# Kernel optimization log

Measured on AMD Instinct MI355X. Metric: run time of the kernel, lower is better.

The kernel has to match this reference:

```python
import jax, jax.numpy as jnp
import numpy as np

EPS = 1e-12  # matches torch F.normalize eps


def setup_inputs() -> dict:
    key = jax.random.key(0)
    k_x, k_w, k_b, k_c, k_f = jax.random.split(key, 5)
    N, C, H, W = 32, 128, 64, 64
    K = 64
    x = jax.random.normal(k_x, (N, C, H, W), dtype=jnp.float32)
    conv_w = jax.random.normal(k_w, (K, C), dtype=jnp.float32) * 0.05  # 1x1 conv weight [K,C,1,1] squeezed
    conv_b = jax.random.normal(k_b, (K,), dtype=jnp.float32) * 0.05
    centroids = jax.random.uniform(k_c, (K, C), dtype=jnp.float32)
    fc_w = jax.random.normal(k_f, (1, K), dtype=jnp.float32) * 0.1  # nn.Linear(K,1,bias=False).weight
    return {"x": x, "conv_w": conv_w, "conv_b": conv_b, "centroids": centroids, "fc_w": fc_w}


def _l2norm(v, axis):
    return v / jnp.maximum(jnp.linalg.norm(v, axis=axis, keepdims=True), EPS)


def reference(x, conv_w, conv_b, centroids, fc_w):
    N, C, H, W = x.shape
    K = conv_w.shape[0]
    # descriptor-wise L2 normalize over channel dim
    x = _l2norm(x, axis=1)
    xf = x.reshape(N, C, H * W)                                   # [N,C,S]
    # 1x1 conv == per-pixel linear over channels
    logits = jnp.einsum('kc,ncs->nks', conv_w, xf) + conv_b[None, :, None]
    a = jax.nn.softmax(logits, axis=1)                            # [N,K,S] soft assignment
    # VLAD: sum_s a[n,k,s] * (x[n,:,s] - centroids[k,:]), loop-free
    vlad = jnp.einsum('nks,ncs->nkc', a, xf) \
           - a.sum(axis=-1)[..., None] * centroids[None, :, :]    # [N,K,C]
    # intra-normalization over descriptor dim
    vlad = _l2norm(vlad, axis=2)
    # lastfc: [N,C,K] @ [K] -> [N,C]
    out = jnp.einsum('nkc,k->nc', vlad, fc_w[0])
    return out
```

## Files before the change

kernel.cpp:

```cpp
#include <hip/hip_runtime.h>
#include <math.h>

#define Nn 32
#define Cc 128
#define Ss 4096
#define Kk 64
#define NCHUNK 32
#define SCHUNK (Ss / NCHUNK)
#define ST 64
#define NSUB (SCHUNK / ST)
#define BLK 256

#define XCS 72
#define XTS 136
#define LKS 68
#define AS  72
#define RS  17

typedef __attribute__((ext_vector_type(8))) short short8;
typedef __attribute__((ext_vector_type(4))) float float4v;

__device__ __forceinline__ unsigned f2bf(float f) {
    unsigned u = __builtin_bit_cast(unsigned, f);
    return (u + 0x7fffu + ((u >> 16) & 1u)) >> 16;
}

__device__ __forceinline__ void bar_lds() {
    asm volatile("s_waitcnt lgkmcnt(0)" ::: "memory");
    __builtin_amdgcn_s_barrier();
    asm volatile("" ::: "memory");
}

__global__ __launch_bounds__(BLK, 3) void netvlad_main(
    const float* __restrict__ x,
    const float* __restrict__ conv_w,
    const float* __restrict__ conv_b,
    float* __restrict__ vladp,
    float* __restrict__ asump,
    float* __restrict__ out)
{
    __shared__ __align__(16) unsigned short xC[Cc * XCS];
    __shared__ __align__(16) float Lbuf[ST * LKS];
    __shared__ __align__(16) unsigned short aB[Kk * AS];
    __shared__ float red[ST * RS];
    __shared__ float invn[ST];
    unsigned short* xT = (unsigned short*)Lbuf;

    const int t     = threadIdx.x;
    const int n     = blockIdx.y;
    const int chunk = blockIdx.x;
    const int w    = t >> 6;
    const int l    = t & 63;
    const int m    = l & 15;
    const int quad = l >> 4;
    const int p    = t >> 2;
    const int ii   = t & 3;

    if (chunk == 0 && n == 0) {
        float4 z4 = make_float4(0.f, 0.f, 0.f, 0.f);
#pragma unroll
        for (int i = 0; i < 4; ++i)
            ((float4*)out)[t + 256 * i] = z4;
    }

    short8 wfrag[4];
    {
        const float* wr_ = conv_w + (16 * w + m) * Cc;
#pragma unroll
        for (int ks = 0; ks < 4; ++ks) {
            float4 wa = *(const float4*)(wr_ + 32 * ks + 8 * quad);
            float4 wb = *(const float4*)(wr_ + 32 * ks + 8 * quad + 4);
            union { short8 s8; unsigned u[4]; } W_;
            W_.u[0] = f2bf(wa.x) | (f2bf(wa.y) << 16);
            W_.u[1] = f2bf(wa.z) | (f2bf(wa.w) << 16);
            W_.u[2] = f2bf(wb.x) | (f2bf(wb.y) << 16);
            W_.u[3] = f2bf(wb.z) | (f2bf(wb.w) << 16);
            wfrag[ks] = W_.s8;
        }
    }
    float bias_r[4];
#pragma unroll
    for (int r = 0; r < 4; ++r) bias_r[r] = conv_b[16 * w + 4 * quad + r];

    float4v acc[8];
#pragma unroll
    for (int nt = 0; nt < 8; ++nt) acc[nt] = (float4v){0.f, 0.f, 0.f, 0.f};
    float asum_part[16];
#pragma unroll
    for (int j = 0; j < 16; ++j) asum_part[j] = 0.f;

    const float* xn = x + (size_t)n * Cc * Ss;

    const int sq   = (t & 15) << 2;
    const int crow = t >> 4;
    const float* xbase = xn + (size_t)(8 * crow) * Ss + chunk * SCHUNK + sq;
    float4 pf[8];
#pragma unroll
    for (int r = 0; r < 8; ++r)
        pf[r] = *(const float4*)(xbase + (size_t)r * Ss);

    for (int sub = 0; sub < NSUB; ++sub) {
        bar_lds();

        {
            unsigned bf[8][4];
            float sp0 = 0.f, sp1 = 0.f, sp2 = 0.f, sp3 = 0.f;
#pragma unroll
            for (int r = 0; r < 8; ++r) {
                float4 v = pf[r];
                sp0 += v.x * v.x; sp1 += v.y * v.y;
                sp2 += v.z * v.z; sp3 += v.w * v.w;
                bf[r][0] = f2bf(v.x); bf[r][1] = f2bf(v.y);
                bf[r][2] = f2bf(v.z); bf[r][3] = f2bf(v.w);
            }
#pragma unroll
            for (int r = 0; r < 8; ++r) {
                uint2 pk = make_uint2(bf[r][0] | (bf[r][1] << 16),
                                      bf[r][2] | (bf[r][3] << 16));
                *(uint2*)&xC[(8 * crow + r) * XCS + sq] = pk;
            }
#pragma unroll
            for (int i = 0; i < 4; ++i) {
                uint4 dd;
                dd.x = bf[0][i] | (bf[1][i] << 16);
                dd.y = bf[2][i] | (bf[3][i] << 16);
                dd.z = bf[4][i] | (bf[5][i] << 16);
                dd.w = bf[6][i] | (bf[7][i] << 16);
                *(uint4*)&xT[(sq + i) * XTS + 8 * crow] = dd;
            }
            red[(sq + 0) * RS + crow] = sp0;
            red[(sq + 1) * RS + crow] = sp1;
            red[(sq + 2) * RS + crow] = sp2;
            red[(sq + 3) * RS + crow] = sp3;
        }
        if (sub < NSUB - 1) {
#pragma unroll
            for (int r = 0; r < 8; ++r)
                pf[r] = *(const float4*)(xbase + (size_t)r * Ss + (sub + 1) * ST);
        }
        bar_lds();

        if (t < ST) {
            float tot = 0.f;
#pragma unroll
            for (int i = 0; i < 16; ++i) tot += red[t * RS + i];
            invn[t] = 1.0f / fmaxf(sqrtf(tot), 1e-12f);
        }
        float4v Lr[4];
#pragma unroll
        for (int nt = 0; nt < 4; ++nt) Lr[nt] = (float4v){0.f, 0.f, 0.f, 0.f};
#pragma unroll
        for (int nt = 0; nt < 4; ++nt) {
#pragma unroll
            for (int ks = 0; ks < 4; ++ks) {
                short8 b = *(const short8*)&xT[(16 * nt + m) * XTS + 32 * ks + 8 * quad];
                Lr[nt] = __builtin_amdgcn_mfma_f32_16x16x32_bf16(wfrag[ks], b, Lr[nt], 0, 0, 0);
            }
        }
        bar_lds();

#pragma unroll
        for (int nt = 0; nt < 4; ++nt) {
            float iv = invn[16 * nt + m];
            float4 o;
            o.x = Lr[nt].x * iv + bias_r[0];
            o.y = Lr[nt].y * iv + bias_r[1];
            o.z = Lr[nt].z * iv + bias_r[2];
            o.w = Lr[nt].w * iv + bias_r[3];
            *(float4*)&Lbuf[(16 * nt + m) * LKS + 16 * w + 4 * quad] = o;
        }
        bar_lds();

        {
            float lv[16];
#pragma unroll
            for (int j = 0; j < 16; ++j) lv[j] = Lbuf[p * LKS + ii + 4 * j];
            float mx = lv[0];
#pragma unroll
            for (int j = 1; j < 16; ++j) mx = fmaxf(mx, lv[j]);
            mx = fmaxf(mx, __shfl_xor(mx, 1));
            mx = fmaxf(mx, __shfl_xor(mx, 2));
            float e[16];
            float lsum = 0.f;
#pragma unroll
            for (int j = 0; j < 16; ++j) { e[j] = __expf(lv[j] - mx); lsum += e[j]; }
            lsum += __shfl_xor(lsum, 1);
            lsum += __shfl_xor(lsum, 2);
            float itot = 1.0f / lsum;
            float sca  = itot * invn[p];
#pragma unroll
            for (int j = 0; j < 16; ++j) {
                float av = e[j] * itot;
                asum_part[j] += av;
                aB[(ii + 4 * j) * AS + p] = (unsigned short)f2bf(e[j] * sca);
            }
        }
        bar_lds();

#pragma unroll
        for (int ks = 0; ks < 2; ++ks) {
            short8 af = *(const short8*)&aB[(16 * w + m) * AS + 32 * ks + 8 * quad];
#pragma unroll
            for (int nt = 0; nt < 8; ++nt) {
                short8 bf_ = *(const short8*)&xC[(16 * nt + m) * XCS + 32 * ks + 8 * quad];
                acc[nt] = __builtin_amdgcn_mfma_f32_16x16x32_bf16(af, bf_, acc[nt], 0, 0, 0);
            }
        }
    }

    {
        float* vb = vladp + ((((size_t)chunk * Nn + n) * Kk) + 16 * w + 4 * quad) * Cc + m;
#pragma unroll
        for (int nt = 0; nt < 8; ++nt) {
            vb[0 * Cc + 16 * nt] = acc[nt].x;
            vb[1 * Cc + 16 * nt] = acc[nt].y;
            vb[2 * Cc + 16 * nt] = acc[nt].z;
            vb[3 * Cc + 16 * nt] = acc[nt].w;
        }
    }

    __syncthreads();
#pragma unroll
    for (int j = 0; j < 16; ++j) Lbuf[p * LKS + ii + 4 * j] = asum_part[j];
    __syncthreads();
    if (t < Kk) {
        float s_ = 0.f;
        for (int p2 = 0; p2 < ST; ++p2) s_ += Lbuf[p2 * LKS + t];
        asump[((size_t)chunk * Nn + n) * Kk + t] = s_;
    }
}

__global__ __launch_bounds__(BLK) void netvlad_final(
    const float* __restrict__ vladp,
    const float* __restrict__ asump,
    const float* __restrict__ centroids,
    const float* __restrict__ fc_w,
    float* __restrict__ out)
{
    __shared__ float asum_s[8];
    __shared__ float scale_s[8];
    __shared__ float4 osum[8 * 32];

    const int t   = threadIdx.x;
    const int bid = blockIdx.x;
    const int n2  = bid >> 3;
    const int kg  = bid & 7;
    const int kl  = t >> 5;
    const int c4  = t & 31;
    const int k2  = 8 * kg + kl;

    float4 v = make_float4(0.f, 0.f, 0.f, 0.f);
    const float* vp = vladp + ((size_t)n2 * Kk + k2) * Cc + 4 * c4;
#pragma unroll
    for (int ch = 0; ch < NCHUNK; ++ch) {
        float4 u = *(const float4*)(vp + (size_t)ch * Nn * Kk * Cc);
        v.x += u.x; v.y += u.y; v.z += u.z; v.w += u.w;
    }
    if (t < 8) {
        float a = 0.f;
#pragma unroll
        for (int ch = 0; ch < NCHUNK; ++ch)
            a += asump[((size_t)ch * Nn + n2) * Kk + 8 * kg + t];
        asum_s[t] = a;
    }
    __syncthreads();

    const float a2 = asum_s[kl];
    float4 cv = *(const float4*)(centroids + (size_t)k2 * Cc + 4 * c4);
    float dx = v.x - a2 * cv.x;
    float dy = v.y - a2 * cv.y;
    float dz = v.z - a2 * cv.z;
    float dw = v.w - a2 * cv.w;

    float ssq = dx * dx + dy * dy + dz * dz + dw * dw;
    ssq += __shfl_xor(ssq, 1);
    ssq += __shfl_xor(ssq, 2);
    ssq += __shfl_xor(ssq, 4);
    ssq += __shfl_xor(ssq, 8);
    ssq += __shfl_xor(ssq, 16);
    if ((t & 31) == 0)
        scale_s[kl] = fc_w[k2] / fmaxf(sqrtf(ssq), 1e-12f);
    __syncthreads();

    const float sc = scale_s[kl];
    osum[kl * 32 + c4] = make_float4(sc * dx, sc * dy, sc * dz, sc * dw);
    __syncthreads();

    if (t < 32) {
        float4 tot = osum[t];
#pragma unroll
        for (int kl2 = 1; kl2 < 8; ++kl2) {
            float4 o2 = osum[kl2 * 32 + t];
            tot.x += o2.x; tot.y += o2.y; tot.z += o2.z; tot.w += o2.w;
        }
        atomicAdd(&out[n2 * Cc + 4 * t + 0], tot.x);
        atomicAdd(&out[n2 * Cc + 4 * t + 1], tot.y);
        atomicAdd(&out[n2 * Cc + 4 * t + 2], tot.z);
        atomicAdd(&out[n2 * Cc + 4 * t + 3], tot.w);
    }
}

extern "C" void kernel_launch(void* const* d_in, const int* in_sizes, int n_in,
                              void* d_out, int out_size, void* d_ws, size_t ws_size,
                              hipStream_t stream) {
    (void)in_sizes; (void)n_in; (void)out_size; (void)ws_size;
    const float* x         = (const float*)d_in[0];
    const float* conv_w    = (const float*)d_in[1];
    const float* conv_b    = (const float*)d_in[2];
    const float* centroids = (const float*)d_in[3];
    const float* fc_w      = (const float*)d_in[4];
    float* out = (float*)d_out;

    float* vladp = (float*)d_ws;
    float* asump = vladp + (size_t)NCHUNK * Nn * Kk * Cc;

    dim3 grid(NCHUNK, Nn);
    netvlad_main<<<grid, BLK, 0, stream>>>(x, conv_w, conv_b, vladp, asump, out);
    netvlad_final<<<dim3(Nn * 8), BLK, 0, stream>>>(vladp, asump, centroids, fc_w, out);
}
```

Measured before the change: 123.7 us.

## Compute full-K logits per wave to drop logit LDS round trip and barriers

Each wave now computes logits for its own 16 spatial positions across all 64 clusters, keeping the whole K dimension in registers. The softmax then reads directly from MFMA accumulators using cross-lane shuffles, which removes the Lbuf staging pass, the separate inverse-norm step and two block barriers per sub-tile. To support this, every thread holds the full conv weight fragments (more registers), occupancy is lowered to 2 blocks per SM, and the spatial chunk count is halved so each block does more sub-tiles.

```diff
diff --git a/kernel.cpp b/kernel.cpp
--- a/kernel.cpp
+++ b/kernel.cpp
@@ -5,7 +5,7 @@
 #define Cc 128
 #define Ss 4096
 #define Kk 64
-#define NCHUNK 32
+#define NCHUNK 16
 #define SCHUNK (Ss / NCHUNK)
 #define ST 64
 #define NSUB (SCHUNK / ST)
@@ -15,7 +15,7 @@
 #define XTS 136
 #define LKS 68
 #define AS  72
-#define RS  17
+#define RS  20
 
 typedef __attribute__((ext_vector_type(8))) short short8;
 typedef __attribute__((ext_vector_type(4))) float float4v;
@@ -25,13 +25,7 @@
     return (u + 0x7fffu + ((u >> 16) & 1u)) >> 16;
 }
 
-__device__ __forceinline__ void bar_lds() {
-    asm volatile("s_waitcnt lgkmcnt(0)" ::: "memory");
-    __builtin_amdgcn_s_barrier();
-    asm volatile("" ::: "memory");
-}
-
-__global__ __launch_bounds__(BLK, 3) void netvlad_main(
+__global__ __launch_bounds__(BLK, 2) void netvlad_main(
     const float* __restrict__ x,
     const float* __restrict__ conv_w,
     const float* __restrict__ conv_b,
@@ -40,11 +34,9 @@
     float* __restrict__ out)
 {
     __shared__ __align__(16) unsigned short xC[Cc * XCS];
-    __shared__ __align__(16) float Lbuf[ST * LKS];
+    __shared__ __align__(16) unsigned short xT[ST * XTS];
     __shared__ __align__(16) unsigned short aB[Kk * AS];
-    __shared__ float red[ST * RS];
-    __shared__ float invn[ST];
-    unsigned short* xT = (unsigned short*)Lbuf;
+    __shared__ __align__(16) float red[ST * RS];
 
     const int t     = threadIdx.x;
     const int n     = blockIdx.y;
@@ -53,8 +45,6 @@
     const int l    = t & 63;
     const int m    = l & 15;
     const int quad = l >> 4;
-    const int p    = t >> 2;
-    const int ii   = t & 3;
 
     if (chunk == 0 && n == 0) {
         float4 z4 = make_float4(0.f, 0.f, 0.f, 0.f);
@@ -63,9 +53,11 @@
             ((float4*)out)[t + 256 * i] = z4;
     }
 
-    short8 wfrag[4];
-    {
-        const float* wr_ = conv_w + (16 * w + m) * Cc;
+    short8 wfragT[4][4];
+    float  bias_s[16];
+#pragma unroll
+    for (int kt = 0; kt < 4; ++kt) {
+        const float* wr_ = conv_w + (16 * kt + m) * Cc;
 #pragma unroll
         for (int ks = 0; ks < 4; ++ks) {
             float4 wa = *(const float4*)(wr_ + 32 * ks + 8 * quad);
@@ -75,12 +67,14 @@
             W_.u[1] = f2bf(wa.z) | (f2bf(wa.w) << 16);
             W_.u[2] = f2bf(wb.x) | (f2bf(wb.y) << 16);
             W_.u[3] = f2bf(wb.z) | (f2bf(wb.w) << 16);
-            wfrag[ks] = W_.s8;
-        }
-    }
-    float bias_r[4];
-#pragma unroll
-    for (int r = 0; r < 4; ++r) bias_r[r] = conv_b[16 * w + 4 * quad + r];
+            wfragT[kt][ks] = W_.s8;
+        }
+        float4 bq = *(const float4*)(conv_b + 16 * kt + 4 * quad);
+        bias_s[4 * kt + 0] = bq.x;
+        bias_s[4 * kt + 1] = bq.y;
+        bias_s[4 * kt + 2] = bq.z;
+        bias_s[4 * kt + 3] = bq.w;
+    }
 
     float4v acc[8];
 #pragma unroll
@@ -99,8 +93,10 @@
     for (int r = 0; r < 8; ++r)
         pf[r] = *(const float4*)(xbase + (size_t)r * Ss);
 
+    const int s_l = 16 * w + m;
+
     for (int sub = 0; sub < NSUB; ++sub) {
-        bar_lds();
+        __syncthreads();
 
         {
             unsigned bf[8][4];
@@ -138,64 +134,68 @@
             for (int r = 0; r < 8; ++r)
                 pf[r] = *(const float4*)(xbase + (size_t)r * Ss + (sub + 1) * ST);
         }
-        bar_lds();
-
-        if (t < ST) {
-            float tot = 0.f;
-#pragma unroll
-            for (int i = 0; i < 16; ++i) tot += red[t * RS + i];
-            invn[t] = 1.0f / fmaxf(sqrtf(tot), 1e-12f);
-        }
-        float4v Lr[4];
-#pragma unroll
-        for (int nt = 0; nt < 4; ++nt) Lr[nt] = (float4v){0.f, 0.f, 0.f, 0.f};
-#pragma unroll
-        for (int nt = 0; nt < 4; ++nt) {
-#pragma unroll
-            for (int ks = 0; ks < 4; ++ks) {
-                short8 b = *(const short8*)&xT[(16 * nt + m) * XTS + 32 * ks + 8 * quad];
-                Lr[nt] = __builtin_amdgcn_mfma_f32_16x16x32_bf16(wfrag[ks], b, Lr[nt], 0, 0, 0);
-            }
-        }
-        bar_lds();
-
-#pragma unroll
-        for (int nt = 0; nt < 4; ++nt) {
-            float iv = invn[16 * nt + m];
-            float4 o;
-            o.x = Lr[nt].x * iv + bias_r[0];
-            o.y = Lr[nt].y * iv + bias_r[1];
-            o.z = Lr[nt].z * iv + bias_r[2];
-            o.w = Lr[nt].w * iv + bias_r[3];
-            *(float4*)&Lbuf[(16 * nt + m) * LKS + 16 * w + 4 * quad] = o;
-        }
-        bar_lds();
+        __syncthreads();
 
         {
+            const float* rp = &red[s_l * RS];
+            float4 q0 = *(const float4*)(rp + 0);
+            float4 q1 = *(const float4*)(rp + 4);
+            float4 q2 = *(const float4*)(rp + 8);
+            float4 q3 = *(const float4*)(rp + 12);
+            float tot = ((q0.x + q0.y) + (q0.z + q0.w))
+                      + ((q1.x + q1.y) + (q1.z + q1.w))
+                      + ((q2.x + q2.y) + (q2.z + q2.w))
+                      + ((q3.x + q3.y) + (q3.z + q3.w));
+            float invl = 1.0f / fmaxf(sqrtf(tot), 1e-12f);
+
+            short8 Bfr[4];
+#pragma unroll
+            for (int ks = 0; ks < 4; ++ks)
+                Bfr[ks] = *(const short8*)&xT[s_l * XTS + 32 * ks + 8 * quad];
+            float4v Lr[4];
+#pragma unroll
+            for (int kt = 0; kt < 4; ++kt) Lr[kt] = (float4v){0.f, 0.f, 0.f, 0.f};
+#pragma unroll
+            for (int kt = 0; kt < 4; ++kt) {
+#pragma unroll
+                for (int ks = 0; ks < 4; ++ks)
+                    Lr[kt] = __builtin_amdgcn_mfma_f32_16x16x32_bf16(
+                        wfragT[kt][ks], Bfr[ks], Lr[kt], 0, 0, 0);
+            }
+
             float lv[16];
 #pragma unroll
-            for (int j = 0; j < 16; ++j) lv[j] = Lbuf[p * LKS + ii + 4 * j];
+            for (int kt = 0; kt < 4; ++kt) {
+                lv[4 * kt + 0] = Lr[kt][0] * invl + bias_s[4 * kt + 0];
+                lv[4 * kt + 1] = Lr[kt][1] * invl + bias_s[4 * kt + 1];
+                lv[4 * kt + 2] = Lr[kt][2] * invl + bias_s[4 * kt + 2];
+                lv[4 * kt + 3] = Lr[kt][3] * invl + bias_s[4 * kt + 3];
+            }
             float mx = lv[0];
 #pragma unroll
             for (int j = 1; j < 16; ++j) mx = fmaxf(mx, lv[j]);
-            mx = fmaxf(mx, __shfl_xor(mx, 1));
-            mx = fmaxf(mx, __shfl_xor(mx, 2));
+            mx = fmaxf(mx, __shfl_xor(mx, 16));
+            mx = fmaxf(mx, __shfl_xor(mx, 32));
             float e[16];
             float lsum = 0.f;
 #pragma unroll
             for (int j = 0; j < 16; ++j) { e[j] = __expf(lv[j] - mx); lsum += e[j]; }
-            lsum += __shfl_xor(lsum, 1);
-            lsum += __shfl_xor(lsum, 2);
+            lsum += __shfl_xor(lsum, 16);
+            lsum += __shfl_xor(lsum, 32);
             float itot = 1.0f / lsum;
-            float sca  = itot * invn[p];
-#pragma unroll
-            for (int j = 0; j < 16; ++j) {
-                float av = e[j] * itot;
-                asum_part[j] += av;
-                aB[(ii + 4 * j) * AS + p] = (unsigned short)f2bf(e[j] * sca);
-            }
-        }
-        bar_lds();
+            float sca  = itot * invl;
+#pragma unroll
+            for (int kt = 0; kt < 4; ++kt) {
+#pragma unroll
+                for (int r = 0; r < 4; ++r) {
+                    float ev = e[4 * kt + r];
+                    asum_part[4 * kt + r] += ev * itot;
+                    aB[(16 * kt + 4 * quad + r) * AS + s_l] =
+                        (unsigned short)f2bf(ev * sca);
+                }
+            }
+        }
+        __syncthreads();
 
 #pragma unroll
         for (int ks = 0; ks < 2; ++ks) {
@@ -220,12 +220,20 @@
     }
 
     __syncthreads();
-#pragma unroll
-    for (int j = 0; j < 16; ++j) Lbuf[p * LKS + ii + 4 * j] = asum_part[j];
+    {
+        float* scr = (float*)xT;
+#pragma unroll
+        for (int kt = 0; kt < 4; ++kt) {
+#pragma unroll
+            for (int r = 0; r < 4; ++r)
+                scr[s_l * LKS + 16 * kt + 4 * quad + r] = asum_part[4 * kt + r];
+        }
+    }
     __syncthreads();
     if (t < Kk) {
+        float* scr = (float*)xT;
         float s_ = 0.f;
-        for (int p2 = 0; p2 < ST; ++p2) s_ += Lbuf[p2 * LKS + t];
+        for (int p2 = 0; p2 < ST; ++p2) s_ += scr[p2 * LKS + t];
         asump[((size_t)chunk * Nn + n) * Kk + t] = s_;
     }
 }
```

After: 118.8 us. 1.04x faster.
